# Kernel tuning notes

Hardware: AMD Instinct MI355X
Metric: run time of the kernel (lower is better)

## Reference

```python
import jax, jax.numpy as jnp
import numpy as np

B, D, K, NUM_CLASSES = 8192, 512, 20, 1024
EPS = 1e-12  # torch F.normalize clamp


def setup_inputs() -> dict:
    key = jax.random.key(0)
    k1, k2 = jax.random.split(key)
    batch = jax.random.normal(k1, (B, D), dtype=jnp.float32)
    labels = jax.random.randint(k2, (B,), 0, NUM_CLASSES, dtype=jnp.int64 if jax.config.jax_enable_x64 else jnp.int32)
    return {"batch": batch, "labels": labels, "k": K}


def reference(batch, labels, k):
    # L2-normalize rows (F.normalize, p=2)
    norm = jnp.maximum(jnp.linalg.norm(batch, axis=1, keepdims=True), EPS)
    x = batch / norm
    cos = x @ x.T                                   # [B, B] cosine similarity
    min_value = cos.min() - 1.0                     # scalar, computed before diag fill
    bs = cos.shape[0]
    diag = jnp.eye(bs, dtype=bool)
    cos = jnp.where(diag, min_value, cos)           # fill_diagonal_(min_value)
    # argsort(-cos)[:, :k]  ==  top-k by similarity (self excluded via diag fill)
    top_vals, top_idx = jax.lax.top_k(cos, k)       # [B, k]
    # preds = (cos + 1)/2 gathered at neighbor indices == (top_vals + 1)/2
    preds = (top_vals + 1.0) * 0.5
    true_labels = (labels[top_idx] == labels[:, None]).astype(jnp.float32)  # [B, k]
    # nn.BCELoss with mean reduction; torch clamps each log term at -100
    logp = jnp.maximum(jnp.log(preds), -100.0)
    log1mp = jnp.maximum(jnp.log1p(-preds), -100.0)
    loss = -(true_labels * logp + (1.0 - true_labels) * log1mp)
    return loss.mean()
```

## Files before the change

### kernel.cpp

```cpp
#include <hip/hip_runtime.h>
#include <hip/hip_bf16.h>

#define NROWS 8192
#define DIM   512
#define KSEL  20
#define PANEL 1024
#define NSURV 512

typedef unsigned int u32;
typedef unsigned long long u64;
typedef short bf16x8 __attribute__((ext_vector_type(8)));
typedef float f32x4 __attribute__((ext_vector_type(4)));
typedef ushort u16x2 __attribute__((ext_vector_type(2)));

typedef const void __attribute__((address_space(1))) as1_void;
typedef void __attribute__((address_space(3))) as3_void;

__device__ __forceinline__ void async_ld16(const ushort* g, ushort* l) {
    __builtin_amdgcn_global_load_lds((as1_void*)g, (as3_void*)l, 16, 0, 0);
}

__device__ __forceinline__ ushort f2bf(float f) {
    u32 u = __float_as_uint(f);
    return (ushort)((u + 0x7FFFu + ((u >> 16) & 1u)) >> 16);
}

__device__ __forceinline__ u32 mono16(u32 r) {
    return r ^ (0x8000u | ((r >> 15) * 0x7FFFu));
}

__device__ __forceinline__ u32 mkey(float f) { return mono16((u32)f2bf(f)); }

__device__ __forceinline__ u32 pkmax(u32 a, u32 b) {
    union { u32 u; u16x2 v; } x, y; x.u = a; y.u = b;
    x.v = __builtin_elementwise_max(x.v, y.v);
    return x.u;
}

__global__ __launch_bounds__(256) void k_norm(const float* __restrict__ x,
                                              ushort* __restrict__ xn) {
    int lane = threadIdx.x & 63;
    int wv   = threadIdx.x >> 6;
    int row  = blockIdx.x * 4 + wv;
    const float4* xr = (const float4*)(x + (size_t)row * DIM);
    float4 a = xr[2 * lane];
    float4 b = xr[2 * lane + 1];
    float ss = a.x*a.x + a.y*a.y + a.z*a.z + a.w*a.w
             + b.x*b.x + b.y*b.y + b.z*b.z + b.w*b.w;
    #pragma unroll
    for (int off = 32; off; off >>= 1) ss += __shfl_xor(ss, off);
    float sc = 1.0f / fmaxf(sqrtf(ss), 1e-12f);
    float v[8] = {a.x*sc, a.y*sc, a.z*sc, a.w*sc, b.x*sc, b.y*sc, b.z*sc, b.w*sc};
    union { ushort u[8]; uint4 q; } o;
    #pragma unroll
    for (int i = 0; i < 8; ++i) o.u[i] = f2bf(v[i]);
    *(uint4*)(xn + (size_t)row * DIM + lane * 8) = o.q;
}

template<bool TRI>
__global__ __launch_bounds__(256) void k_gemm(const ushort* __restrict__ xn,
                                              ushort* __restrict__ C,
                                              ushort* __restrict__ M,
                                              int row0) {
    __shared__ ushort sh[128 * 128];
    ushort* lA = sh;
    ushort* lB = sh + 128 * 64;
    int tid  = threadIdx.x;
    int lane = tid & 63, wv = tid >> 6;
    int wr = wv >> 1, wc = wv & 1;
    int q = lane >> 4, m = lane & 15;
    int bx, by;
    if (TRI) {
        int t = blockIdx.x;
        by = (int)((sqrtf(8.0f * (float)t + 1.0f) - 1.0f) * 0.5f);
        while ((by + 1) * (by + 2) / 2 <= t) ++by;
        while (by * (by + 1) / 2 > t) --by;
        bx = t - by * (by + 1) / 2;
    } else {
        bx = blockIdx.x; by = blockIdx.y;
    }
    int grow0 = row0 + by * 128;
    int gcol0 = bx * 128;
    f32x4 acc[4][4] = {};

    int lr = lane >> 3;
    int lc = lane & 7;
    for (int kc = 0; kc < 8; ++kc) {
        #pragma unroll
        for (int t = 0; t < 4; ++t) {
            int rb  = wv * 32 + t * 8;
            int r   = rb + lr;
            int fch = lc ^ (r & 7);
            async_ld16(xn + (size_t)(grow0 + r) * DIM + kc * 64 + fch * 8, &lA[rb * 64]);
            async_ld16(xn + (size_t)(gcol0 + r) * DIM + kc * 64 + fch * 8, &lB[rb * 64]);
        }
        __syncthreads();
        #pragma unroll
        for (int s = 0; s < 2; ++s) {
            bf16x8 af[4], bfr[4];
            #pragma unroll
            for (int i = 0; i < 4; ++i) {
                int ra = wr * 64 + i * 16 + m;
                af[i]  = *(const bf16x8*)&lA[ra * 64 + (((s * 4 + q) ^ (ra & 7)) * 8)];
                int rb2 = wc * 64 + i * 16 + m;
                bfr[i] = *(const bf16x8*)&lB[rb2 * 64 + (((s * 4 + q) ^ (rb2 & 7)) * 8)];
            }
            #pragma unroll
            for (int i = 0; i < 4; ++i)
                #pragma unroll
                for (int j = 0; j < 4; ++j)
                    acc[i][j] = __builtin_amdgcn_mfma_f32_16x16x32_bf16(af[i], bfr[j], acc[i][j], 0, 0, 0);
        }
        __syncthreads();
    }

    float cmf[4] = {-3.0f, -3.0f, -3.0f, -3.0f};
    #pragma unroll
    for (int i = 0; i < 4; ++i) {
        float rmf[4] = {-3.0f, -3.0f, -3.0f, -3.0f};
        int rloc = wr * 64 + i * 16 + q * 4;
        #pragma unroll
        for (int j = 0; j < 4; ++j) {
            int cl = wc * 64 + j * 16 + m;
            int c  = gcol0 + cl;
            #pragma unroll
            for (int reg = 0; reg < 4; ++reg) {
                int r    = rloc + reg;
                int grw  = row0 + by * 128 + r;
                float a  = acc[i][j][reg];
                bool dg  = (grw == c);
                float mv = dg ? -3.0f : a;
                rmf[reg] = fmaxf(rmf[reg], mv);
                cmf[j]   = fmaxf(cmf[j], mv);
                int D = r * 64 + ((cl >> 1) ^ (q << 3));
                sh[D * 2 + (cl & 1)] = dg ? (ushort)0xC040 : f2bf(a);
            }
        }
        u32 p01 = mkey(rmf[0]) | (mkey(rmf[1]) << 16);
        u32 p23 = mkey(rmf[2]) | (mkey(rmf[3]) << 16);
        #pragma unroll
        for (int off = 1; off <= 8; off <<= 1) {
            p01 = pkmax(p01, (u32)__shfl_xor((int)p01, off));
            p23 = pkmax(p23, (u32)__shfl_xor((int)p23, off));
        }
        if (m == 0) {
            size_t mb = (size_t)(row0 + by * 128 + rloc) * 128 + bx * 2 + wc;
            M[mb]       = (ushort)(p01 & 0xFFFFu);
            M[mb + 128] = (ushort)(p01 >> 16);
            M[mb + 256] = (ushort)(p23 & 0xFFFFu);
            M[mb + 384] = (ushort)(p23 >> 16);
        }
    }
    if (TRI && bx != by) {
        u32 q01 = mkey(cmf[0]) | (mkey(cmf[1]) << 16);
        u32 q23 = mkey(cmf[2]) | (mkey(cmf[3]) << 16);
        q01 = pkmax(q01, (u32)__shfl_xor((int)q01, 16));
        q01 = pkmax(q01, (u32)__shfl_xor((int)q01, 32));
        q23 = pkmax(q23, (u32)__shfl_xor((int)q23, 16));
        q23 = pkmax(q23, (u32)__shfl_xor((int)q23, 32));
        if (q == 0) {
            int gc = gcol0 + wc * 64 + m;
            int sg = by * 2 + wr;
            M[(size_t)(gc +  0) * 128 + sg] = (ushort)(q01 & 0xFFFFu);
            M[(size_t)(gc + 16) * 128 + sg] = (ushort)(q01 >> 16);
            M[(size_t)(gc + 32) * 128 + sg] = (ushort)(q23 & 0xFFFFu);
            M[(size_t)(gc + 48) * 128 + sg] = (ushort)(q23 >> 16);
        }
    }
    __syncthreads();

    int tr = tid >> 4;
    int tc = tid & 15;
    #pragma unroll
    for (int p = 0; p < 8; ++p) {
        int r  = p * 16 + tr;
        int qr = (r >> 2) & 3;
        uint4 v = *(const uint4*)&sh[(r * 64 + ((tc * 4) ^ (qr << 3))) * 2];
        *(uint4*)&C[(size_t)(by * 128 + r) * NROWS + gcol0 + tc * 8] = v;
    }

    if (TRI && bx != by) {
        __syncthreads();
        u32* sh32 = (u32*)sh;
        #pragma unroll
        for (int i = 0; i < 4; ++i) {
            int cd0 = wr * 32 + i * 8 + q * 2;
            #pragma unroll
            for (int j = 0; j < 4; ++j) {
                int rT = wc * 64 + j * 16 + m;
                int gT = ((rT >> 2) & 3) << 3;
                u32 w0 = (u32)f2bf(acc[i][j][0]) | ((u32)f2bf(acc[i][j][1]) << 16);
                u32 w1 = (u32)f2bf(acc[i][j][2]) | ((u32)f2bf(acc[i][j][3]) << 16);
                sh32[rT * 64 + (cd0 ^ gT)]       = w0;
                sh32[rT * 64 + ((cd0 + 1) ^ gT)] = w1;
            }
        }
        __syncthreads();
        #pragma unroll
        for (int p = 0; p < 8; ++p) {
            int ct = p * 16 + tr;
            int gq = ((ct >> 2) & 3) << 3;
            uint4 v = *(const uint4*)&sh32[ct * 64 + ((tc * 4) ^ gq)];
            *(uint4*)&C[(size_t)(gcol0 + ct) * NROWS + by * 128 + tc * 8] = v;
        }
    }
}

__global__ __launch_bounds__(256) void k_select(const ushort* __restrict__ C,
                                                const ushort* __restrict__ M,
                                                const int* __restrict__ labels,
                                                int row0,
                                                float* __restrict__ partials) {
    __shared__ u32 s_surv[4][NSURV];
    __shared__ u32 s_seg[4][128];
    __shared__ u32 s_cnt[4];
    __shared__ u32 s_scnt[4];
    int lane = threadIdx.x & 63;
    int wv   = threadIdx.x >> 6;
    int prow = blockIdx.x * 4 + wv;
    int grow = row0 + prow;
    const ushort* rowC = C + (size_t)prow * NROWS;

    if (lane == 0) { s_cnt[wv] = 0; s_scnt[wv] = 0; }
    __syncthreads();

    u32 pm  = *(const u32*)&M[(size_t)grow * 128 + 2 * lane];
    u32 klo = pm & 0xFFFFu, khi = pm >> 16;

    u32 T = 0;
    #pragma unroll
    for (int b = 15; b >= 0; --b) {
        u32 cand = T | (1u << b);
        int c = __popcll(__ballot(klo >= cand)) + __popcll(__ballot(khi >= cand));
        if (c >= KSEL) T = cand;
    }

    if (klo >= T) { u32 p = atomicAdd(&s_scnt[wv], 1u); s_seg[wv][p] = 2u * lane; }
    if (khi >= T) { u32 p = atomicAdd(&s_scnt[wv], 1u); s_seg[wv][p] = 2u * lane + 1u; }
    u32 nseg = s_scnt[wv];
    int grp = lane >> 3, sub = lane & 7;

    int  sid[4];
    uint4 vv[4];
    #pragma unroll
    for (int t = 0; t < 4; ++t) {
        u32 ix = (u32)(t * 8 + grp);
        sid[t] = (ix < nseg) ? (int)s_seg[wv][ix] : -1;
    }
    #pragma unroll
    for (int t = 0; t < 4; ++t) {
        if (sid[t] >= 0) vv[t] = *(const uint4*)(rowC + sid[t] * 64 + sub * 8);
    }
    #pragma unroll
    for (int t = 0; t < 4; ++t) {
        if (sid[t] < 0) continue;
        u32 wds[4] = { vv[t].x, vv[t].y, vv[t].z, vv[t].w };
        u32 cbase = (u32)(sid[t] * 64 + sub * 8);
        #pragma unroll
        for (int h = 0; h < 4; ++h) {
            u32 w  = wds[h];
            u32 kA = mono16(w & 0xFFFFu);
            u32 kB = mono16(w >> 16);
            if (kA >= T) { u32 p = atomicAdd(&s_cnt[wv], 1u); if (p < NSURV) s_surv[wv][p] = (kA << 16) | (cbase + 2u * h); }
            if (kB >= T) { u32 p = atomicAdd(&s_cnt[wv], 1u); if (p < NSURV) s_surv[wv][p] = (kB << 16) | (cbase + 2u * h + 1u); }
        }
    }
    for (u32 base = 32; base < nseg; base += 8) {
        u32 ix = base + (u32)grp;
        if (ix >= nseg) continue;
        int s = (int)s_seg[wv][ix];
        uint4 v = *(const uint4*)(rowC + s * 64 + sub * 8);
        u32 wds[4] = { v.x, v.y, v.z, v.w };
        u32 cbase = (u32)(s * 64 + sub * 8);
        #pragma unroll
        for (int h = 0; h < 4; ++h) {
            u32 w  = wds[h];
            u32 kA = mono16(w & 0xFFFFu);
            u32 kB = mono16(w >> 16);
            if (kA >= T) { u32 p = atomicAdd(&s_cnt[wv], 1u); if (p < NSURV) s_surv[wv][p] = (kA << 16) | (cbase + 2u * h); }
            if (kB >= T) { u32 p = atomicAdd(&s_cnt[wv], 1u); if (p < NSURV) s_surv[wv][p] = (kB << 16) | (cbase + 2u * h + 1u); }
        }
    }

    u32 cnt = min(s_cnt[wv], (u32)NSURV);
    int mylab = labels[grow];
    float loss = 0.0f;

    if (cnt <= 64u) {
        u32 gg  = ((u32)lane < cnt) ? s_surv[wv][lane] : 0u;
        u32 key = gg >> 16;
        u32 V = 0;
        #pragma unroll
        for (int b = 15; b >= 0; --b) {
            u32 cand = V | (1u << b);
            if (__popcll(__ballot(key >= cand)) >= KSEL) V = cand;
        }
        int cgt  = __popcll(__ballot(key > V));
        int ceq  = __popcll(__ballot(gg != 0 && key == V));
        int need = KSEL - cgt;
        bool incl;
        if (ceq == need) {
            incl = (gg != 0) && (key >= V);
        } else {
            u32 col = gg & 0xFFFFu;
            bool tie = (gg != 0) && (key == V);
            u32 Cv = 0;
            #pragma unroll
            for (int b = 15; b >= 0; --b) {
                u32 cand2 = Cv | (1u << b);
                if (__popcll(__ballot(tie && col >= cand2)) >= need) Cv = cand2;
            }
            incl = (key > V) || (tie && col >= Cv);
        }
        if (incl) {
            u32 col = gg & 0xFFFFu;
            u32 raw = (key & 0x8000u) ? (key ^ 0x8000u) : (key ^ 0xFFFFu);
            float v = __uint_as_float(raw << 16);
            float p = (v + 1.0f) * 0.5f;
            bool tm = (labels[col] == mylab);
            loss -= tm ? fmaxf(logf(p), -100.0f) : fmaxf(log1pf(-p), -100.0f);
        }
    } else {
        u32 g[8];
        #pragma unroll
        for (int j = 0; j < 8; ++j) {
            u32 idx = (u32)lane + (u32)j * 64u;
            g[j] = (idx < cnt) ? s_surv[wv][idx] : 0u;
        }
        u32 V = 0;
        #pragma unroll
        for (int b = 15; b >= 0; --b) {
            u32 cand = V | (1u << b);
            int c = 0;
            #pragma unroll
            for (int j = 0; j < 8; ++j)
                c += __popcll(__ballot((g[j] >> 16) >= cand));
            if (c >= KSEL) V = cand;
        }
        int cgt = 0, ceq = 0;
        #pragma unroll
        for (int j = 0; j < 8; ++j) {
            cgt += __popcll(__ballot(g[j] != 0 && (g[j] >> 16) > V));
            ceq += __popcll(__ballot(g[j] != 0 && (g[j] >> 16) == V));
        }
        int need = KSEL - cgt;
        bool all_ties = (ceq == need);
        #pragma unroll
        for (int j = 0; j < 8; ++j) {
            u32 key = g[j] >> 16, col = g[j] & 0xFFFFu;
            if (g[j] != 0 && (key > V || (all_ties && key == V))) {
                u32 raw = (key & 0x8000u) ? (key ^ 0x8000u) : (key ^ 0xFFFFu);
                float v = __uint_as_float(raw << 16);
                float p = (v + 1.0f) * 0.5f;
                bool tm = (labels[col] == mylab);
                loss -= tm ? fmaxf(logf(p), -100.0f) : fmaxf(log1pf(-p), -100.0f);
            }
        }
        if (!all_ties) {
            for (int r = 0; r < need; ++r) {
                u32 best = 0;
                #pragma unroll
                for (int j = 0; j < 8; ++j) {
                    u32 c2 = (g[j] != 0 && (g[j] >> 16) == V) ? ((g[j] & 0xFFFFu) + 1u) : 0u;
                    best = max(best, c2);
                }
                #pragma unroll
                for (int off = 32; off; off >>= 1) best = max(best, (u32)__shfl_xor((int)best, off));
                #pragma unroll
                for (int j = 0; j < 8; ++j) {
                    if (g[j] != 0 && (g[j] >> 16) == V && ((g[j] & 0xFFFFu) + 1u) == best) {
                        u32 col = g[j] & 0xFFFFu;
                        u32 raw = (V & 0x8000u) ? (V ^ 0x8000u) : (V ^ 0xFFFFu);
                        float v = __uint_as_float(raw << 16);
                        float p = (v + 1.0f) * 0.5f;
                        bool tm = (labels[col] == mylab);
                        loss -= tm ? fmaxf(logf(p), -100.0f) : fmaxf(log1pf(-p), -100.0f);
                        g[j] = 0;
                    }
                }
            }
        }
    }

    #pragma unroll
    for (int off = 32; off; off >>= 1) loss += __shfl_xor(loss, off);
    if (lane == 0) partials[grow] = loss;
}

__global__ __launch_bounds__(256) void k_final(const float* __restrict__ partials,
                                               float* __restrict__ out) {
    __shared__ float s[4];
    int tid = threadIdx.x, lane = tid & 63, wvi = tid >> 6;
    const float4* p4 = (const float4*)partials;
    float sum = 0.0f;
    #pragma unroll
    for (int i = 0; i < 8; ++i) {
        float4 v = p4[tid + i * 256];
        sum += v.x + v.y + v.z + v.w;
    }
    #pragma unroll
    for (int off = 32; off; off >>= 1) sum += __shfl_xor(sum, off);
    if (lane == 0) s[wvi] = sum;
    __syncthreads();
    if (tid == 0) out[0] = (s[0] + s[1] + s[2] + s[3]) * (1.0f / (float)(NROWS * KSEL));
}

extern "C" void kernel_launch(void* const* d_in, const int* in_sizes, int n_in,
                              void* d_out, int out_size, void* d_ws, size_t ws_size,
                              hipStream_t stream) {
    const float* batch  = (const float*)d_in[0];
    const int*   labels = (const int*)d_in[1];

    ushort* xn = (ushort*)d_ws;
    ushort* C  = xn + (size_t)NROWS * DIM;
    ushort* M        = (ushort*)d_in[0];
    float*  partials = (float*)((char*)d_in[0] + (4u << 20));

    size_t need_full = (size_t)NROWS * DIM * 2 + (size_t)NROWS * NROWS * 2;

    k_norm<<<NROWS / 4, 256, 0, stream>>>(batch, xn);

    if (ws_size >= need_full) {
        k_gemm<true><<<dim3(64 * 65 / 2), 256, 0, stream>>>(xn, C, M, 0);
        k_select<<<NROWS / 4, 256, 0, stream>>>(C, M, labels, 0, partials);
    } else {
        for (int p = 0; p < NROWS / PANEL; ++p) {
            k_gemm<false><<<dim3(64, PANEL / 128), 256, 0, stream>>>(xn, C, M, p * PANEL);
            k_select<<<PANEL / 4, 256, 0, stream>>>(C, M, labels, p * PANEL, partials);
        }
    }
    k_final<<<1, 256, 0, stream>>>(partials, (float*)d_out);
}
```

Measured before the change: 164.1 us.

## Write GEMM tile output directly from registers with nontemporal stores

Removes the LDS staging round trip and its barriers in the triangular GEMM epilogue. Each lane now writes its bf16 results straight to global memory: a lane shuffle plus byte permute forms row-major 32-bit words, and 64-bit nontemporal stores write the transposed mirror tile. The diagonal check is gated on a per-tile flag. The triangular tile index is also remapped with a stride-8 swizzle to change block scheduling order. In exchange, the global stores become smaller and less coalesced than the old 16-byte row writes.

```diff
diff --git a/kernel.cpp b/kernel.cpp
--- a/kernel.cpp
+++ b/kernel.cpp
@@ -71,7 +71,8 @@
     int q = lane >> 4, m = lane & 15;
     int bx, by;
     if (TRI) {
-        int t = blockIdx.x;
+        int t = (int)blockIdx.x;
+        t = (t & 7) * 260 + (t >> 3);
         by = (int)((sqrtf(8.0f * (float)t + 1.0f) - 1.0f) * 0.5f);
         while ((by + 1) * (by + 2) / 2 <= t) ++by;
         while (by * (by + 1) / 2 > t) --by;
@@ -114,6 +115,9 @@
         __syncthreads();
     }
 
+    bool isdiag = (row0 + by * 128) == gcol0;
+    u32* Cw = (u32*)C;
+    const int NW = NROWS / 2;
     float cmf[4] = {-3.0f, -3.0f, -3.0f, -3.0f};
     #pragma unroll
     for (int i = 0; i < 4; ++i) {
@@ -123,32 +127,55 @@
         for (int j = 0; j < 4; ++j) {
             int cl = wc * 64 + j * 16 + m;
             int c  = gcol0 + cl;
+            ushort h[4];
             #pragma unroll
             for (int reg = 0; reg < 4; ++reg) {
-                int r    = rloc + reg;
-                int grw  = row0 + by * 128 + r;
                 float a  = acc[i][j][reg];
-                bool dg  = (grw == c);
-                float mv = dg ? -3.0f : a;
+                ushort hb = f2bf(a);
+                float mv = a;
+                if (isdiag && (row0 + by * 128 + rloc + reg) == c) {
+                    hb = (ushort)0xC040;
+                    mv = -3.0f;
+                }
+                h[reg]   = hb;
                 rmf[reg] = fmaxf(rmf[reg], mv);
                 cmf[j]   = fmaxf(cmf[j], mv);
-                int D = r * 64 + ((cl >> 1) ^ (q << 3));
-                sh[D * 2 + (cl & 1)] = dg ? (ushort)0xC040 : f2bf(a);
-            }
-        }
-        u32 p01 = mkey(rmf[0]) | (mkey(rmf[1]) << 16);
-        u32 p23 = mkey(rmf[2]) | (mkey(rmf[3]) << 16);
+            }
+            u32 p01 = (u32)h[0] | ((u32)h[1] << 16);
+            u32 p23 = (u32)h[2] | ((u32)h[3] << 16);
+
+            if (TRI && bx != by) {
+                u64 pk = (u64)p01 | ((u64)p23 << 32);
+                size_t off = (size_t)(gcol0 + cl) * NW + (u32)((by * 128 + rloc) >> 1);
+                __builtin_nontemporal_store(pk, (u64*)(Cw + off));
+            }
+
+            u32 x01 = (u32)__shfl_xor((int)p01, 1);
+            u32 x23 = (u32)__shfl_xor((int)p23, 1);
+            bool odd = (m & 1) != 0;
+            u32 hi = odd ? p23 : x01;
+            u32 lo = odd ? x23 : p01;
+            u32 dA = __builtin_amdgcn_perm(hi, lo, 0x05040100u);
+            u32 dB = __builtin_amdgcn_perm(hi, lo, 0x07060302u);
+            int rA = rloc + (odd ? 2 : 0);
+            size_t cwo = (size_t)(by * 128 + rA) * NW
+                       + (u32)((gcol0 >> 1) + wc * 32 + j * 8 + (m >> 1));
+            __builtin_nontemporal_store(dA, Cw + cwo);
+            __builtin_nontemporal_store(dB, Cw + cwo + NW);
+        }
+        u32 kp01 = mkey(rmf[0]) | (mkey(rmf[1]) << 16);
+        u32 kp23 = mkey(rmf[2]) | (mkey(rmf[3]) << 16);
         #pragma unroll
         for (int off = 1; off <= 8; off <<= 1) {
-            p01 = pkmax(p01, (u32)__shfl_xor((int)p01, off));
-            p23 = pkmax(p23, (u32)__shfl_xor((int)p23, off));
+            kp01 = pkmax(kp01, (u32)__shfl_xor((int)kp01, off));
+            kp23 = pkmax(kp23, (u32)__shfl_xor((int)kp23, off));
         }
         if (m == 0) {
             size_t mb = (size_t)(row0 + by * 128 + rloc) * 128 + bx * 2 + wc;
-            M[mb]       = (ushort)(p01 & 0xFFFFu);
-            M[mb + 128] = (ushort)(p01 >> 16);
-            M[mb + 256] = (ushort)(p23 & 0xFFFFu);
-            M[mb + 384] = (ushort)(p23 >> 16);
+            M[mb]       = (ushort)(kp01 & 0xFFFFu);
+            M[mb + 128] = (ushort)(kp01 >> 16);
+            M[mb + 256] = (ushort)(kp23 & 0xFFFFu);
+            M[mb + 384] = (ushort)(kp23 >> 16);
         }
     }
     if (TRI && bx != by) {
@@ -165,43 +192,6 @@
             M[(size_t)(gc + 16) * 128 + sg] = (ushort)(q01 >> 16);
             M[(size_t)(gc + 32) * 128 + sg] = (ushort)(q23 & 0xFFFFu);
             M[(size_t)(gc + 48) * 128 + sg] = (ushort)(q23 >> 16);
-        }
-    }
-    __syncthreads();
-
-    int tr = tid >> 4;
-    int tc = tid & 15;
-    #pragma unroll
-    for (int p = 0; p < 8; ++p) {
-        int r  = p * 16 + tr;
-        int qr = (r >> 2) & 3;
-        uint4 v = *(const uint4*)&sh[(r * 64 + ((tc * 4) ^ (qr << 3))) * 2];
-        *(uint4*)&C[(size_t)(by * 128 + r) * NROWS + gcol0 + tc * 8] = v;
-    }
-
-    if (TRI && bx != by) {
-        __syncthreads();
-        u32* sh32 = (u32*)sh;
-        #pragma unroll
-        for (int i = 0; i < 4; ++i) {
-            int cd0 = wr * 32 + i * 8 + q * 2;
-            #pragma unroll
-            for (int j = 0; j < 4; ++j) {
-                int rT = wc * 64 + j * 16 + m;
-                int gT = ((rT >> 2) & 3) << 3;
-                u32 w0 = (u32)f2bf(acc[i][j][0]) | ((u32)f2bf(acc[i][j][1]) << 16);
-                u32 w1 = (u32)f2bf(acc[i][j][2]) | ((u32)f2bf(acc[i][j][3]) << 16);
-                sh32[rT * 64 + (cd0 ^ gT)]       = w0;
-                sh32[rT * 64 + ((cd0 + 1) ^ gT)] = w1;
-            }
-        }
-        __syncthreads();
-        #pragma unroll
-        for (int p = 0; p < 8; ++p) {
-            int ct = p * 16 + tr;
-            int gq = ((ct >> 2) & 3) << 3;
-            uint4 v = *(const uint4*)&sh32[ct * 64 + ((tc * 4) ^ gq)];
-            *(uint4*)&C[(size_t)(gcol0 + ct) * NROWS + by * 128 + tc * 8] = v;
         }
     }
 }
```

Measured after the change: 232.9 us. 42.0% more time.
